# Kernel tuning notes

Measured on AMD Instinct MI355X. Metric: run time of the kernel, lower is better.

## Reference

```python
import jax, jax.numpy as jnp
import numpy as np
from jax import lax

K = 3      # reassembly kernel size
UP = 2     # upsample factor


def setup_inputs() -> dict:
    key = jax.random.key(0)
    ks = jax.random.split(key, 4)
    N, C, H, W = 4, 256, 128, 128
    outC = 256
    x = jax.random.normal(ks[0], (N, C, H, W), dtype=jnp.float32)
    w_down = jax.random.normal(ks[1], (C // 4, C), dtype=jnp.float32) * 0.05
    b_down = jnp.zeros((C // 4,), dtype=jnp.float32)
    w_enc = jax.random.normal(ks[2], (UP * UP * K * K, C // 4, K, K), dtype=jnp.float32) * 0.05
    b_enc = jnp.zeros((UP * UP * K * K,), dtype=jnp.float32)
    w_out = jax.random.normal(ks[3], (outC, C), dtype=jnp.float32) * 0.05
    b_out = jnp.zeros((outC,), dtype=jnp.float32)
    return {"x": x, "w_down": w_down, "b_down": b_down,
            "w_enc": w_enc, "b_enc": b_enc, "w_out": w_out, "b_out": b_out}


def _carafe_upsample(x, w_down, b_down, w_enc, b_enc, w_out, b_out):
    N, C, H, W = x.shape
    k2, up2 = K * K, UP * UP
    # kernel prediction branch: 1x1 down conv, 3x3 encoder conv
    t = jnp.einsum('oc,nchw->nohw', w_down, x) + b_down[None, :, None, None]
    enc = lax.conv_general_dilated(
        t, w_enc, window_strides=(1, 1), padding=((K // 2, K // 2), (K // 2, K // 2)),
        dimension_numbers=('NCHW', 'OIHW', 'NCHW')) + b_enc[None, :, None, None]
    # torch encoder channel layout is kk*up2 + ij; pixel_shuffle + softmax(dim=1)
    # + unfold(up,up) is equivalent to softmax over the k^2 axis here.
    enc = enc.reshape(N, k2, up2, H, W)
    kernel = jax.nn.softmax(enc, axis=1)                 # [N,k2,up2,H,W]
    kernel = kernel.transpose(0, 3, 4, 1, 2)             # [N,H,W,k2,up2]
    # extract kxk patches (zero pad), ordering di*K+dj matches torch unfold
    pad = K // 2
    xp = jnp.pad(x, ((0, 0), (0, 0), (pad, pad), (pad, pad)))
    patches = jnp.stack([xp[:, :, di:di + H, dj:dj + W]
                         for di in range(K) for dj in range(K)], axis=-1)  # [N,C,H,W,k2]
    # per-pixel reassembly matmul
    out = jnp.einsum('nchwk,nhwkq->nchwq', patches, kernel)  # [N,C,H,W,up2]
    # pixel_shuffle: channel index c*up2 + i*UP + j -> (h*UP+i, w*UP+j)
    out = out.reshape(N, C, H, W, UP, UP).transpose(0, 1, 2, 4, 3, 5)
    out = out.reshape(N, C, H * UP, W * UP)
    # final 1x1 conv
    return jnp.einsum('oc,nchw->nohw', w_out, out) + b_out[None, :, None, None]


def reference(x, w_down, b_down, w_enc, b_enc, w_out, b_out):
    return _carafe_upsample(x, w_down, b_down, w_enc, b_enc, w_out, b_out)
```

## Files before the change

### kernel.cpp

```cpp
#include <hip/hip_runtime.h>
#include <hip/hip_bf16.h>
#include <stddef.h>

typedef __attribute__((ext_vector_type(8))) short short8;
typedef __attribute__((ext_vector_type(4))) short short4v;
typedef __attribute__((ext_vector_type(4))) unsigned short ushort4v;
typedef __attribute__((ext_vector_type(4))) float floatx4;

#define N_ 4
#define C_ 256
#define H_ 128
#define W_ 128
#define HW_ (H_*W_)
#define NPX_ (N_*HW_)
#define E_ 36
#define OC_ 256

static __device__ __forceinline__ unsigned short f2bf(float f) {
    union { float f; unsigned u; } v; v.f = f;
    unsigned r = v.u + 0x7fff + ((v.u >> 16) & 1);
    return (unsigned short)(r >> 16);
}
static __device__ __forceinline__ float bf2f(unsigned short s) {
    union { unsigned u; float f; } v; v.u = ((unsigned)s) << 16;
    return v.f;
}

__global__ __launch_bounds__(256) void k_prep(const float* __restrict__ wo,
                                              const float* __restrict__ wd,
                                              short* __restrict__ wcomb,
                                              const float* __restrict__ we,
                                              unsigned short* __restrict__ wBT) {
    int bx = blockIdx.x;
    if (bx < 80) {
        int i = (bx * 256 + threadIdx.x) * 4;
        int row = i >> 8, c = i & 255;
        const float* src = (row < 256) ? &wo[row * 256 + c] : &wd[(row - 256) * 256 + c];
        float4 v = *(const float4*)src;
        short4v s;
        s.x = (short)f2bf(v.x); s.y = (short)f2bf(v.y);
        s.z = (short)f2bf(v.z); s.w = (short)f2bf(v.w);
        *(short4v*)&wcomb[i] = s;
    } else {
        int idx = (bx - 80) * 256 + threadIdx.x;
        if (idx < 48 * 576) {
            int e = idx / 576;
            int k = idx - e * 576;
            int tap = k >> 6, c = k & 63;
            float v = (e < E_) ? we[((size_t)e * 64 + c) * 9 + tap] : 0.f;
            wBT[idx] = f2bf(v);
        }
    }
}

__global__ __launch_bounds__(512, 3) void k_gemm(
    const float* __restrict__ x, const short* __restrict__ wcomb,
    const float* __restrict__ bd,
    unsigned short* __restrict__ Gq, unsigned short* __restrict__ t)
{
    __shared__ short Asm[2][320 * 40];
    __shared__ short Bsm[2][128 * 40];

    int tid = threadIdx.x;
    int bx = blockIdx.x;
    int n = bx >> 7;
    int px0 = (bx & 127) * 128;

    int lane = tid & 63;
    int wave = tid >> 6;
    int wm = wave >> 2, wn = wave & 3;

    int ao = tid >> 1, ah = tid & 1;
    int bpx = tid & 127, bcq = tid >> 7;
    bool hasExtra = (tid < 128);

    const float* xb = x + (size_t)n * C_ * HW_ + px0 + bpx;
    const short* wr  = wcomb + ao * C_ + ah * 16;
    const short* wr2 = wcomb + (256 + (tid >> 1)) * C_ + (tid & 1) * 16;

    short8 a0, a1, a2, a3;
    float xg[8];

    auto issue = [&](int c0) {
        a0 = *(const short8*)(wr + c0);
        a1 = *(const short8*)(wr + c0 + 8);
        if (hasExtra) {
            a2 = *(const short8*)(wr2 + c0);
            a3 = *(const short8*)(wr2 + c0 + 8);
        }
        #pragma unroll
        for (int j = 0; j < 8; j++)
            xg[j] = xb[(size_t)(c0 + bcq * 8 + j) * HW_];
    };
    auto commit = [&](int buf) {
        short* ad = &Asm[buf][ao * 40 + ah * 16];
        *(short8*)ad = a0;
        *(short8*)(ad + 8) = a1;
        if (hasExtra) {
            short* ad2 = &Asm[buf][(256 + (tid >> 1)) * 40 + (tid & 1) * 16];
            *(short8*)ad2 = a2;
            *(short8*)(ad2 + 8) = a3;
        }
        short8 bv;
        #pragma unroll
        for (int j = 0; j < 8; j++) bv[j] = (short)f2bf(xg[j]);
        *(short8*)&Bsm[buf][bpx * 40 + bcq * 8] = bv;
    };

    floatx4 acc[10][2];
    #pragma unroll
    for (int fm = 0; fm < 10; fm++) {
        acc[fm][0] = (floatx4)0.f;
        acc[fm][1] = (floatx4)0.f;
    }

    issue(0);
    commit(0);
    __syncthreads();

    for (int kc = 0; kc < 8; kc++) {
        int cur = kc & 1;
        if (kc < 7) issue((kc + 1) * 32);
        short8 bfrag[2];
        #pragma unroll
        for (int fn = 0; fn < 2; fn++) {
            int col = wn * 32 + fn * 16 + (lane & 15);
            bfrag[fn] = *(const short8*)&Bsm[cur][col * 40 + (lane >> 4) * 8];
        }
        #pragma unroll
        for (int fm = 0; fm < 10; fm++) {
            int rbase = (fm < 8) ? (wm * 128 + fm * 16) : (256 + wm * 32 + (fm - 8) * 16);
            int row = rbase + (lane & 15);
            short8 af = *(const short8*)&Asm[cur][row * 40 + (lane >> 4) * 8];
            acc[fm][0] = __builtin_amdgcn_mfma_f32_16x16x32_bf16(af, bfrag[0], acc[fm][0], 0, 0, 0);
            acc[fm][1] = __builtin_amdgcn_mfma_f32_16x16x32_bf16(af, bfrag[1], acc[fm][1], 0, 0, 0);
        }
        if (kc < 7) {
            commit(cur ^ 1);
            __syncthreads();
        }
    }
    #pragma unroll
    for (int fm = 0; fm < 8; fm++) {
        int oq = wm * 32 + fm * 4 + (lane >> 4);
        #pragma unroll
        for (int fn = 0; fn < 2; fn++) {
            int col = px0 + wn * 32 + fn * 16 + (lane & 15);
            ushort4v v;
            v.x = f2bf(acc[fm][fn][0]);
            v.y = f2bf(acc[fm][fn][1]);
            v.z = f2bf(acc[fm][fn][2]);
            v.w = f2bf(acc[fm][fn][3]);
            *(ushort4v*)&Gq[(((size_t)n * 64 + oq) * HW_ + col) * 4] = v;
        }
    }
    #pragma unroll
    for (int f8 = 0; f8 < 2; f8++) {
        int ot = wm * 32 + f8 * 16 + ((lane >> 4) << 2);
        float b0 = bd[ot + 0], b1 = bd[ot + 1], b2 = bd[ot + 2], b3 = bd[ot + 3];
        #pragma unroll
        for (int fn = 0; fn < 2; fn++) {
            int col = px0 + wn * 32 + fn * 16 + (lane & 15);
            ushort4v r;
            r.x = f2bf(acc[8 + f8][fn][0] + b0);
            r.y = f2bf(acc[8 + f8][fn][1] + b1);
            r.z = f2bf(acc[8 + f8][fn][2] + b2);
            r.w = f2bf(acc[8 + f8][fn][3] + b3);
            *(ushort4v*)&t[((size_t)n * HW_ + col) * 64 + ot] = r;
        }
    }
}

__global__ __launch_bounds__(256) void k_enc(
    const unsigned short* __restrict__ t, const unsigned short* __restrict__ wBT,
    const float* __restrict__ be, float* __restrict__ kern)
{
    __shared__ short Tl[390 * 64];
    float* El = (float*)Tl;

    int bx = blockIdx.x;
    int n = bx >> 7, h = bx & 127;
    int tid = threadIdx.x;
    int lane = tid & 63, wave = tid >> 6;

    short8 bpre[3][3];
    const unsigned short* wB0 = wBT + (size_t)(lane & 15) * 576 + (lane >> 4) * 8;
    #pragma unroll
    for (int p = 0; p < 2; p++)
        #pragma unroll
        for (int fn = 0; fn < 3; fn++)
            bpre[p][fn] = *(const short8*)(wB0 + fn * 16 * 576 + p * 32);

    for (int idx = tid; idx < 3120; idx += 256) {
        int r = idx >> 3, ch = idx & 7;
        int di = r / 130, rr = r - di * 130;
        int hh = h + di - 1, ww = rr - 1;
        short8 v = {0,0,0,0,0,0,0,0};
        if (hh >= 0 && hh < H_ && ww >= 0 && ww < W_)
            v = *(const short8*)&t[((size_t)(n * H_ + hh) * W_ + ww) * 64 + ch * 8];
        int us = (r * 64 + ch * 8) ^ ((r & 7) << 3);
        *(short8*)&Tl[us] = v;
    }
    __syncthreads();

    floatx4 acc[2][3];
    #pragma unroll
    for (int mf = 0; mf < 2; mf++)
        #pragma unroll
        for (int fn = 0; fn < 3; fn++)
            acc[mf][fn] = (floatx4)0.f;

    int pxw = wave * 32 + (lane & 15);
    int kq = (lane >> 4) * 8;

    #pragma unroll
    for (int kc = 0; kc < 18; kc++) {
        if (kc < 16) {
            int slot = (kc + 2) % 3;
            #pragma unroll
            for (int fn = 0; fn < 3; fn++)
                bpre[slot][fn] = *(const short8*)(wB0 + fn * 16 * 576 + (kc + 2) * 32);
        }
        const int cur = kc % 3;
        const int tap = kc >> 1, chalf = kc & 1;
        const int di = tap / 3, dj = tap % 3;
        #pragma unroll
        for (int mf = 0; mf < 2; mf++) {
            int r = di * 130 + pxw + mf * 16 + dj;
            int us = (r * 64 + chalf * 32 + kq) ^ ((r & 7) << 3);
            short8 af = *(const short8*)&Tl[us];
            #pragma unroll
            for (int fn = 0; fn < 3; fn++)
                acc[mf][fn] = __builtin_amdgcn_mfma_f32_16x16x32_bf16(af, bpre[cur][fn], acc[mf][fn], 0, 0, 0);
        }
    }
    __syncthreads();

    #pragma unroll
    for (int mf = 0; mf < 2; mf++)
        #pragma unroll
        for (int fn = 0; fn < 3; fn++)
            #pragma unroll
            for (int i = 0; i < 4; i++) {
                int px = wave * 32 + mf * 16 + (lane >> 4) * 4 + i;
                El[px * 49 + fn * 16 + (lane & 15)] = acc[mf][fn][i];
            }
    __syncthreads();

    int sp = tid >> 1;
    int pxg = n * HW_ + h * W_ + sp;
    #pragma unroll
    for (int qq = 0; qq < 2; qq++) {
        int q = (tid & 1) * 2 + qq;
        float l[9];
        #pragma unroll
        for (int k = 0; k < 9; k++) l[k] = El[sp * 49 + k * 4 + q] + be[k * 4 + q];
        float m = l[0];
        #pragma unroll
        for (int k = 1; k < 9; k++) m = fmaxf(m, l[k]);
        float ex[9], s = 0.f;
        #pragma unroll
        for (int k = 0; k < 9; k++) { ex[k] = __expf(l[k] - m); s += ex[k]; }
        float inv = 1.f / s;
        #pragma unroll
        for (int k = 0; k < 9; k++)
            kern[(size_t)(k * 4 + q) * NPX_ + pxg] = ex[k] * inv;
    }
}

__global__ __launch_bounds__(256) void k_up(
    const unsigned short* __restrict__ Gq, const float* __restrict__ kern,
    const float* __restrict__ bo, float* __restrict__ y)
{
    int bx = blockIdx.x;
    int x7 = bx & 7;
    int g  = bx >> 3;
    int hbhi = g & 7;
    int og = (g >> 3) & 7;
    int n  = g >> 6;
    int hb = hbhi * 8 + x7;

    int tid = threadIdx.x;
    int h = hb * 2 + (tid >> 7);
    int w = tid & 127;
    int idxp = n * HW_ + h * W_ + w;

    float kv[36];
    #pragma unroll
    for (int e = 0; e < E_; e++)
        kv[e] = kern[(size_t)e * NPX_ + idxp];

    int off[9]; bool val[9];
    #pragma unroll
    for (int di = 0; di < 3; di++) {
        int hh = h + di - 1;
        bool hvv = (hh >= 0 && hh < H_);
        int hc = hvv ? hh : h;
        #pragma unroll
        for (int dj = 0; dj < 3; dj++) {
            int ww = w + dj - 1;
            bool wvv = (ww >= 0 && ww < W_);
            int wc = wvv ? ww : w;
            off[di * 3 + dj] = hc * W_ + wc;
            val[di * 3 + dj] = hvv && wvv;
        }
    }

    const unsigned short* Gb = Gq + ((size_t)n * 64 + og * 8) * HW_ * 4;
    size_t ybase = ((size_t)n * OC_ + og * 32) * (4 * HW_) + (size_t)(2 * h) * 256 + 2 * w;

    #pragma unroll 2
    for (int j = 0; j < 8; j++) {
        const unsigned short* Gj = Gb + (size_t)j * HW_ * 4;
        float b0 = bo[og * 32 + j * 4 + 0];
        float b1 = bo[og * 32 + j * 4 + 1];
        float b2 = bo[og * 32 + j * 4 + 2];
        float b3 = bo[og * 32 + j * 4 + 3];
        float a[4][4];
        #pragma unroll
        for (int s = 0; s < 4; s++) { a[0][s] = b0; a[1][s] = b1; a[2][s] = b2; a[3][s] = b3; }
        #pragma unroll
        for (int k = 0; k < 9; k++) {
            ushort4v gv = *(const ushort4v*)(Gj + (size_t)off[k] * 4);
            float g0 = val[k] ? bf2f(gv.x) : 0.f;
            float g1 = val[k] ? bf2f(gv.y) : 0.f;
            float g2 = val[k] ? bf2f(gv.z) : 0.f;
            float g3 = val[k] ? bf2f(gv.w) : 0.f;
            #pragma unroll
            for (int s = 0; s < 4; s++) {
                float kw = kv[k * 4 + s];
                a[0][s] = fmaf(g0, kw, a[0][s]);
                a[1][s] = fmaf(g1, kw, a[1][s]);
                a[2][s] = fmaf(g2, kw, a[2][s]);
                a[3][s] = fmaf(g3, kw, a[3][s]);
            }
        }
        #pragma unroll
        for (int i = 0; i < 4; i++) {
            float* yp = y + ybase + (size_t)(j * 4 + i) * (4 * HW_);
            float2 r0; r0.x = a[i][0]; r0.y = a[i][1];
            float2 r1; r1.x = a[i][2]; r1.y = a[i][3];
            *(float2*)yp = r0;
            *(float2*)(yp + 256) = r1;
        }
    }
}

extern "C" void kernel_launch(void* const* d_in, const int* in_sizes, int n_in,
                              void* d_out, int out_size, void* d_ws, size_t ws_size,
                              hipStream_t stream) {
    const float* x  = (const float*)d_in[0];
    const float* wd = (const float*)d_in[1];
    const float* bd = (const float*)d_in[2];
    const float* we = (const float*)d_in[3];
    const float* be = (const float*)d_in[4];
    const float* wo = (const float*)d_in[5];
    const float* bo = (const float*)d_in[6];
    float* y = (float*)d_out;

    unsigned short* t = (unsigned short*)d_ws;
    float* kern = (float*)(t + (size_t)NPX_ * 64);
    short* wcomb = (short*)(kern + (size_t)E_ * NPX_);
    unsigned short* wBT = (unsigned short*)(wcomb + (size_t)320 * C_);
    unsigned short* Gq  = wBT + (size_t)48 * 576;

    k_prep<<<188,  256, 0, stream>>>(wo, wd, wcomb, we, wBT);
    k_gemm<<<512,  512, 0, stream>>>(x, wcomb, bd, Gq, t);
    k_enc <<<512,  256, 0, stream>>>(t, wBT, be, kern);
    k_up  <<<2048, 256, 0, stream>>>(Gq, kern, bo, y);
}
```

Baseline: 138.8 us.

## Shrink GEMM pixel tile, load weights directly to registers, store softmax kernels in bf16

The 1x1-conv GEMM now uses 64-pixel tiles across 1024 blocks and drops the shared-memory staging of weights. Each wave loads its A fragments straight from global memory into registers with a one-step prefetch, and x loads are double-buffered two steps ahead. The softmax reassembly kernels are written and read as bf16 rather than fp32, which halves that intermediate's traffic between k_enc and k_up. The trade-offs are more global and L2 reads of the weights per block, and a further small precision loss in the kernel weights.

```diff
diff --git a/kernel.cpp b/kernel.cpp
--- a/kernel.cpp
+++ b/kernel.cpp
@@ -53,127 +53,124 @@
     }
 }
 
-__global__ __launch_bounds__(512, 3) void k_gemm(
+__global__ __launch_bounds__(512, 4) void k_gemm(
     const float* __restrict__ x, const short* __restrict__ wcomb,
     const float* __restrict__ bd,
     unsigned short* __restrict__ Gq, unsigned short* __restrict__ t)
 {
-    __shared__ short Asm[2][320 * 40];
-    __shared__ short Bsm[2][128 * 40];
+    __shared__ short Bsm[2][64 * 40];
 
     int tid = threadIdx.x;
     int bx = blockIdx.x;
-    int n = bx >> 7;
-    int px0 = (bx & 127) * 128;
+    int n = bx >> 8;
+    int px0 = (bx & 255) * 64;
 
     int lane = tid & 63;
     int wave = tid >> 6;
-    int wm = wave >> 2, wn = wave & 3;
-
-    int ao = tid >> 1, ah = tid & 1;
-    int bpx = tid & 127, bcq = tid >> 7;
-    bool hasExtra = (tid < 128);
-
+    int wm = wave >> 1, wn = wave & 1;
+
+    int bpx = tid & 63, bcq = tid >> 6;
     const float* xb = x + (size_t)n * C_ * HW_ + px0 + bpx;
-    const short* wr  = wcomb + ao * C_ + ah * 16;
-    const short* wr2 = wcomb + (256 + (tid >> 1)) * C_ + (tid & 1) * 16;
-
-    short8 a0, a1, a2, a3;
-    float xg[8];
-
-    auto issue = [&](int c0) {
-        a0 = *(const short8*)(wr + c0);
-        a1 = *(const short8*)(wr + c0 + 8);
-        if (hasExtra) {
-            a2 = *(const short8*)(wr2 + c0);
-            a3 = *(const short8*)(wr2 + c0 + 8);
-        }
-        #pragma unroll
-        for (int j = 0; j < 8; j++)
-            xg[j] = xb[(size_t)(c0 + bcq * 8 + j) * HW_];
+
+    int aoff[5];
+    #pragma unroll
+    for (int fm = 0; fm < 5; fm++) {
+        int row = wm * 80 + fm * 16 + (lane & 15);
+        aoff[fm] = row * 256 + ((lane >> 4) << 3);
+    }
+
+    float xs[2][4];
+    short8 aw[5], an[5];
+
+    auto xload = [&](int c0, int slot) {
+        #pragma unroll
+        for (int j = 0; j < 4; j++)
+            xs[slot][j] = xb[(size_t)(c0 + bcq * 4 + j) * HW_];
     };
-    auto commit = [&](int buf) {
-        short* ad = &Asm[buf][ao * 40 + ah * 16];
-        *(short8*)ad = a0;
-        *(short8*)(ad + 8) = a1;
-        if (hasExtra) {
-            short* ad2 = &Asm[buf][(256 + (tid >> 1)) * 40 + (tid & 1) * 16];
-            *(short8*)ad2 = a2;
-            *(short8*)(ad2 + 8) = a3;
-        }
-        short8 bv;
-        #pragma unroll
-        for (int j = 0; j < 8; j++) bv[j] = (short)f2bf(xg[j]);
-        *(short8*)&Bsm[buf][bpx * 40 + bcq * 8] = bv;
+    auto commit = [&](int buf, int slot) {
+        short4v bv;
+        bv.x = (short)f2bf(xs[slot][0]);
+        bv.y = (short)f2bf(xs[slot][1]);
+        bv.z = (short)f2bf(xs[slot][2]);
+        bv.w = (short)f2bf(xs[slot][3]);
+        *(short4v*)&Bsm[buf][bpx * 40 + bcq * 4] = bv;
     };
 
-    floatx4 acc[10][2];
-    #pragma unroll
-    for (int fm = 0; fm < 10; fm++) {
+    floatx4 acc[5][2];
+    #pragma unroll
+    for (int fm = 0; fm < 5; fm++) {
         acc[fm][0] = (floatx4)0.f;
         acc[fm][1] = (floatx4)0.f;
     }
 
-    issue(0);
-    commit(0);
+    xload(0, 0);
+    #pragma unroll
+    for (int fm = 0; fm < 5; fm++)
+        aw[fm] = *(const short8*)&wcomb[aoff[fm]];
+    commit(0, 0);
+    xload(32, 1);
     __syncthreads();
 
+    #pragma unroll
     for (int kc = 0; kc < 8; kc++) {
         int cur = kc & 1;
-        if (kc < 7) issue((kc + 1) * 32);
-        short8 bfrag[2];
+        if (kc < 6) xload((kc + 2) * 32, kc & 1);
+        if (kc < 7) {
+            #pragma unroll
+            for (int fm = 0; fm < 5; fm++)
+                an[fm] = *(const short8*)&wcomb[aoff[fm] + (kc + 1) * 32];
+        }
         #pragma unroll
         for (int fn = 0; fn < 2; fn++) {
             int col = wn * 32 + fn * 16 + (lane & 15);
-            bfrag[fn] = *(const short8*)&Bsm[cur][col * 40 + (lane >> 4) * 8];
-        }
-        #pragma unroll
-        for (int fm = 0; fm < 10; fm++) {
-            int rbase = (fm < 8) ? (wm * 128 + fm * 16) : (256 + wm * 32 + (fm - 8) * 16);
-            int row = rbase + (lane & 15);
-            short8 af = *(const short8*)&Asm[cur][row * 40 + (lane >> 4) * 8];
-            acc[fm][0] = __builtin_amdgcn_mfma_f32_16x16x32_bf16(af, bfrag[0], acc[fm][0], 0, 0, 0);
-            acc[fm][1] = __builtin_amdgcn_mfma_f32_16x16x32_bf16(af, bfrag[1], acc[fm][1], 0, 0, 0);
+            short8 bf = *(const short8*)&Bsm[cur][col * 40 + (lane >> 4) * 8];
+            #pragma unroll
+            for (int fm = 0; fm < 5; fm++)
+                acc[fm][fn] = __builtin_amdgcn_mfma_f32_16x16x32_bf16(aw[fm], bf, acc[fm][fn], 0, 0, 0);
         }
         if (kc < 7) {
-            commit(cur ^ 1);
+            commit(cur ^ 1, (kc + 1) & 1);
+            #pragma unroll
+            for (int fm = 0; fm < 5; fm++) aw[fm] = an[fm];
             __syncthreads();
         }
     }
-    #pragma unroll
-    for (int fm = 0; fm < 8; fm++) {
-        int oq = wm * 32 + fm * 4 + (lane >> 4);
-        #pragma unroll
-        for (int fn = 0; fn < 2; fn++) {
-            int col = px0 + wn * 32 + fn * 16 + (lane & 15);
-            ushort4v v;
-            v.x = f2bf(acc[fm][fn][0]);
-            v.y = f2bf(acc[fm][fn][1]);
-            v.z = f2bf(acc[fm][fn][2]);
-            v.w = f2bf(acc[fm][fn][3]);
-            *(ushort4v*)&Gq[(((size_t)n * 64 + oq) * HW_ + col) * 4] = v;
-        }
-    }
-    #pragma unroll
-    for (int f8 = 0; f8 < 2; f8++) {
-        int ot = wm * 32 + f8 * 16 + ((lane >> 4) << 2);
-        float b0 = bd[ot + 0], b1 = bd[ot + 1], b2 = bd[ot + 2], b3 = bd[ot + 3];
-        #pragma unroll
-        for (int fn = 0; fn < 2; fn++) {
-            int col = px0 + wn * 32 + fn * 16 + (lane & 15);
-            ushort4v r;
-            r.x = f2bf(acc[8 + f8][fn][0] + b0);
-            r.y = f2bf(acc[8 + f8][fn][1] + b1);
-            r.z = f2bf(acc[8 + f8][fn][2] + b2);
-            r.w = f2bf(acc[8 + f8][fn][3] + b3);
-            *(ushort4v*)&t[((size_t)n * HW_ + col) * 64 + ot] = r;
+
+    #pragma unroll
+    for (int fm = 0; fm < 5; fm++) {
+        int row0 = wm * 80 + fm * 16;
+        if (row0 < 256) {
+            int oq = (row0 >> 2) + (lane >> 4);
+            #pragma unroll
+            for (int fn = 0; fn < 2; fn++) {
+                int col = px0 + wn * 32 + fn * 16 + (lane & 15);
+                ushort4v v;
+                v.x = f2bf(acc[fm][fn][0]);
+                v.y = f2bf(acc[fm][fn][1]);
+                v.z = f2bf(acc[fm][fn][2]);
+                v.w = f2bf(acc[fm][fn][3]);
+                *(ushort4v*)&Gq[(((size_t)n * 64 + oq) * HW_ + col) * 4] = v;
+            }
+        } else {
+            int ot = row0 - 256 + ((lane >> 4) << 2);
+            float b0 = bd[ot + 0], b1 = bd[ot + 1], b2 = bd[ot + 2], b3 = bd[ot + 3];
+            #pragma unroll
+            for (int fn = 0; fn < 2; fn++) {
+                int col = px0 + wn * 32 + fn * 16 + (lane & 15);
+                ushort4v r;
+                r.x = f2bf(acc[fm][fn][0] + b0);
+                r.y = f2bf(acc[fm][fn][1] + b1);
+                r.z = f2bf(acc[fm][fn][2] + b2);
+                r.w = f2bf(acc[fm][fn][3] + b3);
+                *(ushort4v*)&t[((size_t)n * HW_ + col) * 64 + ot] = r;
+            }
         }
     }
 }
 
 __global__ __launch_bounds__(256) void k_enc(
     const unsigned short* __restrict__ t, const unsigned short* __restrict__ wBT,
-    const float* __restrict__ be, float* __restrict__ kern)
+    const float* __restrict__ be, unsigned short* __restrict__ kernb)
 {
     __shared__ short Tl[390 * 64];
     float* El = (float*)Tl;
@@ -264,12 +261,12 @@
         float inv = 1.f / s;
         #pragma unroll
         for (int k = 0; k < 9; k++)
-            kern[(size_t)(k * 4 + q) * NPX_ + pxg] = ex[k] * inv;
+            kernb[(size_t)(k * 4 + q) * NPX_ + pxg] = f2bf(ex[k] * inv);
     }
 }
 
 __global__ __launch_bounds__(256) void k_up(
-    const unsigned short* __restrict__ Gq, const float* __restrict__ kern,
+    const unsigned short* __restrict__ Gq, const unsigned short* __restrict__ kernb,
     const float* __restrict__ bo, float* __restrict__ y)
 {
     int bx = blockIdx.x;
@@ -288,7 +285,7 @@
     float kv[36];
     #pragma unroll
     for (int e = 0; e < E_; e++)
-        kv[e] = kern[(size_t)e * NPX_ + idxp];
+        kv[e] = bf2f(kernb[(size_t)e * NPX_ + idxp]);
 
     int off[9]; bool val[9];
     #pragma unroll
@@ -359,13 +356,13 @@
     float* y = (float*)d_out;
 
     unsigned short* t = (unsigned short*)d_ws;
-    float* kern = (float*)(t + (size_t)NPX_ * 64);
-    short* wcomb = (short*)(kern + (size_t)E_ * NPX_);
+    unsigned short* kernb = t + (size_t)NPX_ * 64;
+    short* wcomb = (short*)(kernb + (size_t)E_ * NPX_);
     unsigned short* wBT = (unsigned short*)(wcomb + (size_t)320 * C_);
     unsigned short* Gq  = wBT + (size_t)48 * 576;
 
     k_prep<<<188,  256, 0, stream>>>(wo, wd, wcomb, we, wBT);
-    k_gemm<<<512,  512, 0, stream>>>(x, wcomb, bd, Gq, t);
-    k_enc <<<512,  256, 0, stream>>>(t, wBT, be, kern);
-    k_up  <<<2048, 256, 0, stream>>>(Gq, kern, bo, y);
-}
+    k_gemm<<<1024, 512, 0, stream>>>(x, wcomb, bd, Gq, t);
+    k_enc <<<512,  256, 0, stream>>>(t, wBT, be, kernb);
+    k_up  <<<2048, 256, 0, stream>>>(Gq, kernb, bo, y);
+}
```

Measured after the change: 136.4 us. About the same (-1.7%).
